# Performance work log

Hardware: AMD Instinct MI355X
Metric: run time of the kernel (lower is better)

## Reference

```python
import jax, jax.numpy as jnp
import numpy as np

B = 8192   # batch
S = 16     # n_dims = len(dims_in)
E = 256    # embedding_dim
H = 8      # heads
FF = 1024  # feedforward_dim
L = 6      # transformer_layers
V = 512    # max_dim (vocab per slot)
U = 1024   # mlp_units
DC = 64    # dims_c
LN_EPS = 1e-5


def setup_inputs() -> dict:
    key = jax.random.key(0)
    ks = iter(jax.random.split(key, 40))
    s = 0.02
    def p(shape):
        return jax.random.normal(next(ks), shape, jnp.float32) * s
    return dict(
        x=jax.random.randint(next(ks), (B, S), 0, V, dtype=jnp.int32),
        c=jax.random.normal(next(ks), (B, DC), jnp.float32),
        x_emb=p((V, E)),
        pos_emb=p((S, E)),
        c_W=p((E, DC)), c_b=jnp.zeros((E,), jnp.float32),
        Wqkv=p((L, 3 * E, E)), bqkv=jnp.zeros((L, 3 * E), jnp.float32),
        Wo=p((L, E, E)), bo=jnp.zeros((L, E), jnp.float32),
        ln1_g=jnp.ones((L, E), jnp.float32), ln1_b=jnp.zeros((L, E), jnp.float32),
        W1=p((L, FF, E)), b1=jnp.zeros((L, FF), jnp.float32),
        W2=p((L, E, FF)), b2=jnp.zeros((L, E), jnp.float32),
        ln2_g=jnp.ones((L, E), jnp.float32), ln2_b=jnp.zeros((L, E), jnp.float32),
        mW0=p((U, E)), mb0=jnp.zeros((U,), jnp.float32),
        mW1=p((U, U)), mb1=jnp.zeros((U,), jnp.float32),
        mW2=p((V, U)), mb2=jnp.zeros((V,), jnp.float32),
    )


def _ln(x, g, b):
    mu = x.mean(-1, keepdims=True)
    var = ((x - mu) ** 2).mean(-1, keepdims=True)
    return (x - mu) * jax.lax.rsqrt(var + LN_EPS) * g + b


def reference(x, c, x_emb, pos_emb, c_W, c_b, Wqkv, bqkv, Wo, bo,
              ln1_g, ln1_b, W1, b1, W2, b2, ln2_g, ln2_b,
              mW0, mb0, mW1, mb1, mW2, mb2):
    Bn = x.shape[0]
    dh = E // H
    # x_embed = pad(x_embedding(x[:, :-1]), one zero timestep at front)
    xe = jnp.pad(x_emb[x[:, :-1]], ((0, 0), (1, 0), (0, 0)))  # [B,S,E]
    h = xe + pos_emb[None] + (c @ c_W.T + c_b)[:, None, :]
    causal = jnp.triu(jnp.ones((S, S), bool), 1)  # True = masked
    for l in range(L):  # post-norm TransformerEncoderLayer, dropout=0, gelu
        qkv = h @ Wqkv[l].T + bqkv[l]
        q, k, v = jnp.split(qkv, 3, axis=-1)
        q = q.reshape(Bn, S, H, dh)
        k = k.reshape(Bn, S, H, dh)
        v = v.reshape(Bn, S, H, dh)
        sc = jnp.einsum('bshd,bthd->bhst', q, k) / np.sqrt(dh).astype(np.float32)
        sc = jnp.where(causal[None, None], jnp.float32(-1e30), sc)
        a = jax.nn.softmax(sc, axis=-1)
        o = jnp.einsum('bhst,bthd->bshd', a, v).reshape(Bn, S, E)
        h = _ln(h + o @ Wo[l].T + bo[l], ln1_g[l], ln1_b[l])
        f = jax.nn.gelu(h @ W1[l].T + b1[l], approximate=False) @ W2[l].T + b2[l]
        h = _ln(h + f, ln2_g[l], ln2_b[l])
    # MLP head: 3 linear layers with ReLU
    z = jax.nn.relu(h @ mW0.T + mb0)
    z = jax.nn.relu(z @ mW1.T + mb1)
    logits = z @ mW2.T + mb2  # [B,S,V]
    # prior_mask is all ones since dims_in[i] == max_dim for all i
    pu = jnp.exp(logits)
    picked = jnp.take_along_axis(pu, x[:, :, None], axis=2)[:, :, 0]
    prob = jnp.prod(picked / pu.sum(axis=2), axis=1)
    return jnp.log(prob)
```

## Files before the change

### kernel.cpp

```cpp
#include <hip/hip_runtime.h>
#include <hip/hip_bf16.h>
#include <math.h>

#define B_  8192
#define S_  16
#define E_  256
#define H_  8
#define FF_ 1024
#define L_  6
#define V_  512
#define U_  1024
#define DC_ 64
#define M_  (B_ * S_)

typedef __attribute__((ext_vector_type(8))) short short8;
typedef __attribute__((ext_vector_type(4))) float f32x4;

__device__ __forceinline__ float wave_sum(float v) {
#pragma unroll
  for (int off = 32; off >= 1; off >>= 1) v += __shfl_xor(v, off);
  return v;
}
__device__ __forceinline__ float wave_max(float v) {
#pragma unroll
  for (int off = 32; off >= 1; off >>= 1) v = fmaxf(v, __shfl_xor(v, off));
  return v;
}

__device__ __forceinline__ unsigned bfround(float f) {
  unsigned u = __builtin_bit_cast(unsigned, f);
  return (u + 0x7FFFu + ((u >> 16) & 1u)) >> 16;
}
__device__ __forceinline__ unsigned pack2(float lo, float hi) {
  return bfround(lo) | (bfround(hi) << 16);
}
__device__ __forceinline__ float b2f(short s) {
  return __builtin_bit_cast(float, (unsigned)(unsigned short)s << 16);
}
__device__ __forceinline__ float blo(unsigned u) { return __builtin_bit_cast(float, u << 16); }
__device__ __forceinline__ float bhi(unsigned u) { return __builtin_bit_cast(float, u & 0xFFFF0000u); }

__device__ __forceinline__ void gload_lds16(const void* g, void* l) {
  __builtin_amdgcn_global_load_lds(
      (const __attribute__((address_space(1))) void*)g,
      (__attribute__((address_space(3))) void*)l, 16, 0, 0);
}

__device__ __forceinline__ int xcd_swz(int bid, int nblk) {
  return (bid & 7) * (nblk >> 3) + (bid >> 3);
}

__global__ void w2bf_kernel(const float* __restrict__ src, short* __restrict__ dst) {
  const int i = blockIdx.x * 256 + threadIdx.x;
  const float4 v = ((const float4*)src)[i];
  uint2 p;
  p.x = pack2(v.x, v.y);
  p.y = pack2(v.z, v.w);
  ((uint2*)dst)[i] = p;
}

template <int ACT, bool RES, bool OUTF32>
__launch_bounds__(256, 2)
__global__ void gemm_bf16_kernel(const short* __restrict__ A, const short* __restrict__ W,
                                 const float* __restrict__ bias, const short* __restrict__ res,
                                 void* __restrict__ Cv, int M, int N, int K) {
  __shared__ __align__(16) short As[128 * 64];
  __shared__ __align__(16) short Ws[128 * 64];
  const int t  = threadIdx.x;
  const int w  = t >> 6;
  const int l  = t & 63;
  const int wr = w >> 1;
  const int wc = w & 1;
  const int lr = l & 15;
  const int kg = l >> 4;
  const int nbn = N / 128;
  const int bid = xcd_swz(blockIdx.x, gridDim.x);
  const int bm = bid / nbn;
  const int bn = bid % nbn;
  const int m0 = bm * 128, n0 = bn * 128;

  f32x4 acc[4][4] = {};

  const int rg = l >> 3;
  const int cs = ((l & 7) ^ rg) * 8;
  const int swz = (lr & 7) * 8;

  for (int k0 = 0; k0 < K; k0 += 64) {
    const short* Ab = &A[(size_t)m0 * K + k0 + cs];
    const short* Wb = &W[(size_t)n0 * K + k0 + cs];
#pragma unroll
    for (int q = 0; q < 4; ++q) {
      const int i = w * 4 + q;
      const int row = i * 8 + rg;
      gload_lds16(Ab + (size_t)row * K, &As[i * 512]);
      gload_lds16(Wb + (size_t)row * K, &Ws[i * 512]);
    }
    __syncthreads();

#pragma unroll
    for (int kk = 0; kk < 64; kk += 32) {
      short8 af[4], bf[4];
#pragma unroll
      for (int mi = 0; mi < 4; ++mi)
        af[mi] = *(const short8*)&As[(wr * 64 + mi * 16 + lr) * 64 + ((kk + kg * 8) ^ swz)];
#pragma unroll
      for (int ni = 0; ni < 4; ++ni)
        bf[ni] = *(const short8*)&Ws[(wc * 64 + ni * 16 + lr) * 64 + ((kk + kg * 8) ^ swz)];
#pragma unroll
      for (int mi = 0; mi < 4; ++mi)
#pragma unroll
        for (int ni = 0; ni < 4; ++ni)
          acc[mi][ni] = __builtin_amdgcn_mfma_f32_16x16x32_bf16(af[mi], bf[ni], acc[mi][ni], 0, 0, 0);
    }
    __syncthreads();
  }

  float* Cf = (float*)Cv;
  short* Cb = (short*)Cv;
#pragma unroll
  for (int ni = 0; ni < 4; ++ni) {
    const int n = n0 + wc * 64 + ni * 16 + lr;
    const float bv = bias[n];
#pragma unroll
    for (int mi = 0; mi < 4; ++mi) {
      const int mbase = m0 + wr * 64 + mi * 16 + kg * 4;
#pragma unroll
      for (int j = 0; j < 4; ++j) {
        float z = acc[mi][ni][j] + bv;
        const size_t off = (size_t)(mbase + j) * N + n;
        if (RES) z += b2f(res[off]);
        if (ACT == 1) z = 0.5f * z * (1.0f + erff(z * 0.70710678118654752f));
        if (ACT == 2) z = fmaxf(z, 0.0f);
        if (OUTF32) Cf[off] = z;
        else        Cb[off] = (short)bfround(z);
      }
    }
  }
}

__launch_bounds__(256, 2)
__global__ void gemm_ln_kernel(const short* __restrict__ A, const short* __restrict__ W,
                               const float* __restrict__ bias, const short* __restrict__ res,
                               const float* __restrict__ g, const float* __restrict__ bb,
                               short* __restrict__ out, int M, int K) {
  __shared__ __align__(16) short As[64 * 64];
  __shared__ __align__(16) short Ws[256 * 64];
  __shared__ float lnbuf[64][2][2];
  const int t  = threadIdx.x;
  const int w  = t >> 6;
  const int l  = t & 63;
  const int wr = w >> 1;
  const int wc = w & 1;
  const int lr = l & 15;
  const int kg = l >> 4;
  const int bid = xcd_swz(blockIdx.x, gridDim.x);
  const int m0 = bid * 64;

  f32x4 acc[2][8] = {};

  const int rg = l >> 3;
  const int cs = ((l & 7) ^ rg) * 8;
  const int swz = (lr & 7) * 8;

  for (int k0 = 0; k0 < K; k0 += 64) {
    const short* Ab = &A[(size_t)m0 * K + k0 + cs];
    const short* Wb = &W[(size_t)0 * K + k0 + cs];
#pragma unroll
    for (int q = 0; q < 2; ++q) {
      const int i = w * 2 + q;
      gload_lds16(Ab + (size_t)(i * 8 + rg) * K, &As[i * 512]);
    }
#pragma unroll
    for (int q = 0; q < 8; ++q) {
      const int i = w * 8 + q;
      gload_lds16(Wb + (size_t)(i * 8 + rg) * K, &Ws[i * 512]);
    }
    __syncthreads();

#pragma unroll
    for (int kk = 0; kk < 64; kk += 32) {
      short8 af[2], bf[8];
#pragma unroll
      for (int mi = 0; mi < 2; ++mi)
        af[mi] = *(const short8*)&As[(wr * 32 + mi * 16 + lr) * 64 + ((kk + kg * 8) ^ swz)];
#pragma unroll
      for (int ni = 0; ni < 8; ++ni)
        bf[ni] = *(const short8*)&Ws[(wc * 128 + ni * 16 + lr) * 64 + ((kk + kg * 8) ^ swz)];
#pragma unroll
      for (int mi = 0; mi < 2; ++mi)
#pragma unroll
        for (int ni = 0; ni < 8; ++ni)
          acc[mi][ni] = __builtin_amdgcn_mfma_f32_16x16x32_bf16(af[mi], bf[ni], acc[mi][ni], 0, 0, 0);
    }
    __syncthreads();
  }

  float biasv[8], gv[8], bv[8];
#pragma unroll
  for (int ni = 0; ni < 8; ++ni) {
    const int n = wc * 128 + ni * 16 + lr;
    biasv[ni] = bias[n]; gv[ni] = g[n]; bv[ni] = bb[n];
  }
  float ps1[2][4] = {}, ps2[2][4] = {};
#pragma unroll
  for (int mi = 0; mi < 2; ++mi)
#pragma unroll
    for (int j = 0; j < 4; ++j) {
      const int m = m0 + wr * 32 + mi * 16 + kg * 4 + j;
#pragma unroll
      for (int ni = 0; ni < 8; ++ni) {
        const int n = wc * 128 + ni * 16 + lr;
        float z = acc[mi][ni][j] + biasv[ni] + b2f(res[(size_t)m * 256 + n]);
        acc[mi][ni][j] = z;
        ps1[mi][j] += z;
        ps2[mi][j] = fmaf(z, z, ps2[mi][j]);
      }
    }
#pragma unroll
  for (int off = 1; off <= 8; off <<= 1) {
#pragma unroll
    for (int mi = 0; mi < 2; ++mi)
#pragma unroll
      for (int j = 0; j < 4; ++j) {
        ps1[mi][j] += __shfl_xor(ps1[mi][j], off);
        ps2[mi][j] += __shfl_xor(ps2[mi][j], off);
      }
  }
  if (lr == 0) {
#pragma unroll
    for (int mi = 0; mi < 2; ++mi)
#pragma unroll
      for (int j = 0; j < 4; ++j) {
        const int r = wr * 32 + mi * 16 + kg * 4 + j;
        lnbuf[r][wc][0] = ps1[mi][j];
        lnbuf[r][wc][1] = ps2[mi][j];
      }
  }
  __syncthreads();

#pragma unroll
  for (int mi = 0; mi < 2; ++mi)
#pragma unroll
    for (int j = 0; j < 4; ++j) {
      const int r = wr * 32 + mi * 16 + kg * 4 + j;
      const float s1 = lnbuf[r][0][0] + lnbuf[r][1][0];
      const float s2 = lnbuf[r][0][1] + lnbuf[r][1][1];
      const float mu  = s1 * (1.0f / 256.0f);
      const float var = s2 * (1.0f / 256.0f) - mu * mu;
      const float rs  = 1.0f / sqrtf(var + 1e-5f);
      const size_t mrow = (size_t)(m0 + r) * 256;
#pragma unroll
      for (int ni = 0; ni < 8; ++ni) {
        const int n = wc * 128 + ni * 16 + lr;
        out[mrow + n] = (short)bfround((acc[mi][ni][j] - mu) * rs * gv[ni] + bv[ni]);
      }
    }
}

__global__ void embed_kernel(const int* __restrict__ x, const float* __restrict__ x_emb,
                             const float* __restrict__ pos_emb, const float* __restrict__ cproj,
                             short* __restrict__ h, int b0) {
  const int idx = blockIdx.x * 256 + threadIdx.x;
  const int e4 = idx & 63;
  const int s  = (idx >> 6) & 15;
  const int b  = b0 + (idx >> 10);
  const float4 pe = ((const float4*)pos_emb)[s * 64 + e4];
  const float4 cp = ((const float4*)cproj)[b * 64 + e4];
  float4 v;
  v.x = pe.x + cp.x; v.y = pe.y + cp.y; v.z = pe.z + cp.z; v.w = pe.w + cp.w;
  if (s > 0) {
    const int tok = x[b * 16 + s - 1];
    const float4 xe = ((const float4*)x_emb)[tok * 64 + e4];
    v.x += xe.x; v.y += xe.y; v.z += xe.z; v.w += xe.w;
  }
  uint2 p;
  p.x = pack2(v.x, v.y);
  p.y = pack2(v.z, v.w);
  ((uint2*)h)[idx] = p;
}

__launch_bounds__(256)
__global__ void attn_kernel(const short* __restrict__ qkv, short* __restrict__ o) {
  __shared__ __align__(16) float sq[4][16][36];
  __shared__ __align__(16) float sk[4][16][36];
  __shared__ __align__(16) float sv[4][16][36];
  __shared__ float sa[4][16][17];
  const int w   = threadIdx.x >> 6;
  const int l   = threadIdx.x & 63;
  const int gid = blockIdx.x * 4 + w;
  const int b   = gid >> 3;
  const int hh  = gid & 7;

  {
    const int s  = l >> 2;
    const int d0 = (l & 3) * 8;
    const size_t base = (size_t)(b * 16 + s) * 768 + hh * 32 + d0;
    const uint4 qv = *(const uint4*)&qkv[base];
    const uint4 kv = *(const uint4*)&qkv[base + 256];
    const uint4 vv = *(const uint4*)&qkv[base + 512];
    float* dq = &sq[w][s][d0];
    float* dk = &sk[w][s][d0];
    float* dv = &sv[w][s][d0];
    dq[0] = blo(qv.x); dq[1] = bhi(qv.x); dq[2] = blo(qv.y); dq[3] = bhi(qv.y);
    dq[4] = blo(qv.z); dq[5] = bhi(qv.z); dq[6] = blo(qv.w); dq[7] = bhi(qv.w);
    dk[0] = blo(kv.x); dk[1] = bhi(kv.x); dk[2] = blo(kv.y); dk[3] = bhi(kv.y);
    dk[4] = blo(kv.z); dk[5] = bhi(kv.z); dk[6] = blo(kv.w); dk[7] = bhi(kv.w);
    dv[0] = blo(vv.x); dv[1] = bhi(vv.x); dv[2] = blo(vv.y); dv[3] = bhi(vv.y);
    dv[4] = blo(vv.z); dv[5] = bhi(vv.z); dv[6] = blo(vv.w); dv[7] = bhi(vv.w);
  }
  __syncthreads();

  {
    const int sr = l & 15;
    const int tq = l >> 4;
    float sc[4] = {0.f, 0.f, 0.f, 0.f};
    for (int d = 0; d < 32; d += 4) {
      const float4 qv = *(const float4*)&sq[w][sr][d];
#pragma unroll
      for (int j = 0; j < 4; ++j) {
        const float4 kv = *(const float4*)&sk[w][tq * 4 + j][d];
        sc[j] += qv.x * kv.x + qv.y * kv.y + qv.z * kv.z + qv.w * kv.w;
      }
    }
    float mx = -1e30f;
#pragma unroll
    for (int j = 0; j < 4; ++j) {
      const int tt = tq * 4 + j;
      sc[j] = (tt > sr) ? -1e30f : sc[j] * 0.17677669529663687f;
      mx = fmaxf(mx, sc[j]);
    }
    mx = fmaxf(mx, __shfl_xor(mx, 16));
    mx = fmaxf(mx, __shfl_xor(mx, 32));
    float e[4]; float sm = 0.f;
#pragma unroll
    for (int j = 0; j < 4; ++j) { e[j] = expf(sc[j] - mx); sm += e[j]; }
    sm += __shfl_xor(sm, 16);
    sm += __shfl_xor(sm, 32);
#pragma unroll
    for (int j = 0; j < 4; ++j) sa[w][sr][tq * 4 + j] = e[j] / sm;
  }
  __syncthreads();

  {
    const int s  = l >> 2;
    const int d0 = (l & 3) * 8;
    float a0[4] = {0.f, 0.f, 0.f, 0.f}, a1[4] = {0.f, 0.f, 0.f, 0.f};
    for (int tt = 0; tt < 16; ++tt) {
      const float av = sa[w][s][tt];
      const float4 v0 = *(const float4*)&sv[w][tt][d0];
      const float4 v1 = *(const float4*)&sv[w][tt][d0 + 4];
      a0[0] = fmaf(av, v0.x, a0[0]); a0[1] = fmaf(av, v0.y, a0[1]);
      a0[2] = fmaf(av, v0.z, a0[2]); a0[3] = fmaf(av, v0.w, a0[3]);
      a1[0] = fmaf(av, v1.x, a1[0]); a1[1] = fmaf(av, v1.y, a1[1]);
      a1[2] = fmaf(av, v1.z, a1[2]); a1[3] = fmaf(av, v1.w, a1[3]);
    }
    const size_t ob = (size_t)(b * 16 + s) * 256 + hh * 32 + d0;
    uint4 p;
    p.x = pack2(a0[0], a0[1]); p.y = pack2(a0[2], a0[3]);
    p.z = pack2(a1[0], a1[1]); p.w = pack2(a1[2], a1[3]);
    *(uint4*)&o[ob] = p;
  }
}

__launch_bounds__(256)
__global__ void logprob_kernel(const float* __restrict__ logits, const int* __restrict__ x,
                               float* __restrict__ out, int b0) {
  const int w  = threadIdx.x >> 6;
  const int l  = threadIdx.x & 63;
  const int bl = blockIdx.x * 4 + w;
  const int b  = b0 + bl;
  float acc = 0.f;
  for (int s = 0; s < 16; ++s) {
    const float* row = logits + (size_t)(bl * 16 + s) * 512;
    float v[8];
#pragma unroll
    for (int i = 0; i < 8; ++i) v[i] = row[l + 64 * i];
    float mx = v[0];
#pragma unroll
    for (int i = 1; i < 8; ++i) mx = fmaxf(mx, v[i]);
    mx = wave_max(mx);
    float se = 0.f;
#pragma unroll
    for (int i = 0; i < 8; ++i) se += expf(v[i] - mx);
    se = wave_sum(se);
    const float lse = mx + logf(se);
    const float picked = row[x[b * 16 + s]];
    acc += picked - lse;
  }
  if (l == 0) out[b] = acc;
}

extern "C" void kernel_launch(void* const* d_in, const int* in_sizes, int n_in,
                              void* d_out, int out_size, void* d_ws, size_t ws_size,
                              hipStream_t stream) {
  const int*   x       = (const int*)  d_in[0];
  const float* c       = (const float*)d_in[1];
  const float* x_emb   = (const float*)d_in[2];
  const float* pos_emb = (const float*)d_in[3];
  const float* c_W     = (const float*)d_in[4];
  const float* c_b     = (const float*)d_in[5];
  const float* Wqkv    = (const float*)d_in[6];
  const float* bqkv    = (const float*)d_in[7];
  const float* Wo      = (const float*)d_in[8];
  const float* bo      = (const float*)d_in[9];
  const float* ln1_g   = (const float*)d_in[10];
  const float* ln1_b   = (const float*)d_in[11];
  const float* W1      = (const float*)d_in[12];
  const float* b1      = (const float*)d_in[13];
  const float* W2      = (const float*)d_in[14];
  const float* b2      = (const float*)d_in[15];
  const float* ln2_g   = (const float*)d_in[16];
  const float* ln2_b   = (const float*)d_in[17];
  const float* mW0     = (const float*)d_in[18];
  const float* mb0     = (const float*)d_in[19];
  const float* mW1     = (const float*)d_in[20];
  const float* mb1     = (const float*)d_in[21];
  const float* mW2     = (const float*)d_in[22];
  const float* mb2     = (const float*)d_in[23];
  float* out = (float*)d_out;

  const size_t nWqkv = (size_t)L_ * 768 * 256;
  const size_t nWo   = (size_t)L_ * 256 * 256;
  const size_t nW1   = (size_t)L_ * 1024 * 256;
  const size_t nW2   = (size_t)L_ * 256 * 1024;
  const size_t nmW0  = (size_t)U_ * E_;
  const size_t nmW1  = (size_t)U_ * U_;
  const size_t nmW2  = (size_t)V_ * U_;
  const size_t ncW   = (size_t)E_ * DC_;
  const size_t nC    = (size_t)B_ * DC_;
  const size_t WBF   = nWqkv + nWo + nW1 + nW2 + nmW0 + nmW1 + nmW2 + ncW + nC;

  short* bWqkv = (short*)d_ws;
  short* bWo   = bWqkv + nWqkv;
  short* bW1   = bWo   + nWo;
  short* bW2   = bW1   + nW1;
  short* bmW0  = bW2   + nW2;
  short* bmW1  = bmW0  + nmW0;
  short* bmW2  = bmW1  + nmW1;
  short* bcW   = bmW2  + nmW2;
  short* bC    = bcW   + ncW;

  const size_t fixed_bytes = WBF * 2 + (size_t)B_ * 256 * 4;
  int BC = 0;
  for (int bc = B_; bc >= 128; bc >>= 1) {
    const size_t need = fixed_bytes + (size_t)bc * 16 * 2304 * 2;
    if (need <= ws_size) { BC = bc; break; }
  }
  if (BC == 0) return;
  const int MC = BC * 16;
  const int NCHUNK = B_ / BC;

  float* cpr = (float*)((char*)d_ws + WBF * 2);
  short* h   = (short*)(cpr + (size_t)B_ * 256);
  short* R   = h + (size_t)MC * 256;
  short* X   = R + (size_t)MC * 1024;
  float* logitsF = (float*)R;

  const dim3 blk(256);

  w2bf_kernel<<<dim3(nWqkv / 1024), blk, 0, stream>>>(Wqkv, bWqkv);
  w2bf_kernel<<<dim3(nWo   / 1024), blk, 0, stream>>>(Wo,   bWo);
  w2bf_kernel<<<dim3(nW1   / 1024), blk, 0, stream>>>(W1,   bW1);
  w2bf_kernel<<<dim3(nW2   / 1024), blk, 0, stream>>>(W2,   bW2);
  w2bf_kernel<<<dim3(nmW0  / 1024), blk, 0, stream>>>(mW0,  bmW0);
  w2bf_kernel<<<dim3(nmW1  / 1024), blk, 0, stream>>>(mW1,  bmW1);
  w2bf_kernel<<<dim3(nmW2  / 1024), blk, 0, stream>>>(mW2,  bmW2);
  w2bf_kernel<<<dim3(ncW   / 1024), blk, 0, stream>>>(c_W,  bcW);
  w2bf_kernel<<<dim3(nC    / 1024), blk, 0, stream>>>(c,    bC);

  gemm_bf16_kernel<0, false, true><<<dim3((B_ / 128) * (E_ / 128)), blk, 0, stream>>>(
      bC, bcW, c_b, nullptr, cpr, B_, E_, DC_);

  for (int ci = 0; ci < NCHUNK; ++ci) {
    const int b0 = ci * BC;
    embed_kernel<<<dim3((MC * 64) / 256), blk, 0, stream>>>(x, x_emb, pos_emb, cpr, h, b0);

    for (int l = 0; l < L_; ++l) {
      gemm_bf16_kernel<0, false, false><<<dim3((MC / 128) * (768 / 128)), blk, 0, stream>>>(
          h, bWqkv + (size_t)l * 768 * 256, bqkv + (size_t)l * 768, nullptr, R, MC, 768, 256);
      attn_kernel<<<dim3(BC * 2), blk, 0, stream>>>(R, X);
      gemm_ln_kernel<<<dim3(MC / 64), blk, 0, stream>>>(
          X, bWo + (size_t)l * 256 * 256, bo + (size_t)l * 256, h,
          ln1_g + (size_t)l * 256, ln1_b + (size_t)l * 256, h, MC, 256);
      gemm_bf16_kernel<1, false, false><<<dim3((MC / 128) * (FF_ / 128)), blk, 0, stream>>>(
          h, bW1 + (size_t)l * 1024 * 256, b1 + (size_t)l * 1024, nullptr, R, MC, 1024, 256);
      gemm_ln_kernel<<<dim3(MC / 64), blk, 0, stream>>>(
          R, bW2 + (size_t)l * 256 * 1024, b2 + (size_t)l * 256, h,
          ln2_g + (size_t)l * 256, ln2_b + (size_t)l * 256, h, MC, 1024);
    }

    gemm_bf16_kernel<2, false, false><<<dim3((MC / 128) * (U_ / 128)), blk, 0, stream>>>(
        h, bmW0, mb0, nullptr, R, MC, U_, E_);
    gemm_bf16_kernel<2, false, false><<<dim3((MC / 128) * (U_ / 128)), blk, 0, stream>>>(
        R, bmW1, mb1, nullptr, X, MC, U_, U_);
    gemm_bf16_kernel<0, false, true><<<dim3((MC / 128) * (V_ / 128)), blk, 0, stream>>>(
        X, bmW2, mb2, nullptr, logitsF, MC, V_, U_);

    logprob_kernel<<<dim3(BC / 4), blk, 0, stream>>>(logitsF, x, out, b0);
  }
}
```

Baseline: 3.841 ms.

## Fuse causal attention into the Wo projection + residual + LayerNorm kernel

Attention for a 64-row tile (4 sequences, all 8 heads) is now computed in shared memory inside the output-projection GEMM kernel. The per-head outputs are written into a swizzled LDS buffer that feeds the MFMA loop directly. This removes a separate attention launch and the global round-trip of the attention output tensor. In exchange, the attention phase runs head by head with three block barriers per head, and the LDS footprint grows, which may limit occupancy.

```diff
diff --git a/kernel.cpp b/kernel.cpp
--- a/kernel.cpp
+++ b/kernel.cpp
@@ -257,6 +257,200 @@
     }
 }
 
+__launch_bounds__(256, 2)
+__global__ void attn_wo_ln_kernel(const short* __restrict__ qkv, const short* __restrict__ W,
+                                  const float* __restrict__ bias, const short* __restrict__ res,
+                                  const float* __restrict__ g, const float* __restrict__ bb,
+                                  short* __restrict__ out, int M) {
+  __shared__ __align__(16) short oS[64 * 256];
+  __shared__ __align__(16) short Ws[256 * 64];
+  __shared__ float lnbuf[64][2][2];
+  const int t  = threadIdx.x;
+  const int w  = t >> 6;
+  const int l  = t & 63;
+  const int wr = w >> 1;
+  const int wc = w & 1;
+  const int lr = l & 15;
+  const int kg = l >> 4;
+  const int bid = xcd_swz(blockIdx.x, gridDim.x);
+  const int m0 = bid * 64;
+
+  {
+    float* scr = (float*)Ws;
+    float* sq = scr + w * 2048;
+    float* sk = sq + 576;
+    float* sv = sq + 1152;
+    float* sa = sq + 1728;
+    const int s  = l >> 2;
+    const int d0 = (l & 3) * 8;
+    const int sr = l & 15;
+    const int tq = l >> 4;
+
+    for (int hh = 0; hh < 8; ++hh) {
+      {
+        const size_t base = (size_t)(m0 + w * 16 + s) * 768 + hh * 32 + d0;
+        const uint4 qv = *(const uint4*)&qkv[base];
+        const uint4 kv = *(const uint4*)&qkv[base + 256];
+        const uint4 vv = *(const uint4*)&qkv[base + 512];
+        float* dq = &sq[s * 36 + d0];
+        float* dk = &sk[s * 36 + d0];
+        float* dv = &sv[s * 36 + d0];
+        dq[0] = blo(qv.x); dq[1] = bhi(qv.x); dq[2] = blo(qv.y); dq[3] = bhi(qv.y);
+        dq[4] = blo(qv.z); dq[5] = bhi(qv.z); dq[6] = blo(qv.w); dq[7] = bhi(qv.w);
+        dk[0] = blo(kv.x); dk[1] = bhi(kv.x); dk[2] = blo(kv.y); dk[3] = bhi(kv.y);
+        dk[4] = blo(kv.z); dk[5] = bhi(kv.z); dk[6] = blo(kv.w); dk[7] = bhi(kv.w);
+        dv[0] = blo(vv.x); dv[1] = bhi(vv.x); dv[2] = blo(vv.y); dv[3] = bhi(vv.y);
+        dv[4] = blo(vv.z); dv[5] = bhi(vv.z); dv[6] = blo(vv.w); dv[7] = bhi(vv.w);
+      }
+      __syncthreads();
+      {
+        float sc[4] = {0.f, 0.f, 0.f, 0.f};
+        for (int d = 0; d < 32; d += 4) {
+          const float4 qv = *(const float4*)&sq[sr * 36 + d];
+#pragma unroll
+          for (int j = 0; j < 4; ++j) {
+            const float4 kv = *(const float4*)&sk[(tq * 4 + j) * 36 + d];
+            sc[j] += qv.x * kv.x + qv.y * kv.y + qv.z * kv.z + qv.w * kv.w;
+          }
+        }
+        float mx = -1e30f;
+#pragma unroll
+        for (int j = 0; j < 4; ++j) {
+          const int tt = tq * 4 + j;
+          sc[j] = (tt > sr) ? -1e30f : sc[j] * 0.17677669529663687f;
+          mx = fmaxf(mx, sc[j]);
+        }
+        mx = fmaxf(mx, __shfl_xor(mx, 16));
+        mx = fmaxf(mx, __shfl_xor(mx, 32));
+        float e[4]; float sm = 0.f;
+#pragma unroll
+        for (int j = 0; j < 4; ++j) { e[j] = expf(sc[j] - mx); sm += e[j]; }
+        sm += __shfl_xor(sm, 16);
+        sm += __shfl_xor(sm, 32);
+#pragma unroll
+        for (int j = 0; j < 4; ++j) sa[sr * 17 + tq * 4 + j] = e[j] / sm;
+      }
+      __syncthreads();
+      {
+        float a0[4] = {0.f, 0.f, 0.f, 0.f}, a1[4] = {0.f, 0.f, 0.f, 0.f};
+        for (int tt = 0; tt < 16; ++tt) {
+          const float av = sa[s * 17 + tt];
+          const float4 v0 = *(const float4*)&sv[tt * 36 + d0];
+          const float4 v1 = *(const float4*)&sv[tt * 36 + d0 + 4];
+          a0[0] = fmaf(av, v0.x, a0[0]); a0[1] = fmaf(av, v0.y, a0[1]);
+          a0[2] = fmaf(av, v0.z, a0[2]); a0[3] = fmaf(av, v0.w, a0[3]);
+          a1[0] = fmaf(av, v1.x, a1[0]); a1[1] = fmaf(av, v1.y, a1[1]);
+          a1[2] = fmaf(av, v1.z, a1[2]); a1[3] = fmaf(av, v1.w, a1[3]);
+        }
+        const int r = w * 16 + s;
+        const int cphys = (hh * 32 + d0) ^ ((r & 7) * 8);
+        uint4 p;
+        p.x = pack2(a0[0], a0[1]); p.y = pack2(a0[2], a0[3]);
+        p.z = pack2(a1[0], a1[1]); p.w = pack2(a1[2], a1[3]);
+        *(uint4*)&oS[r * 256 + cphys] = p;
+      }
+      __syncthreads();
+    }
+  }
+
+  f32x4 acc[2][8] = {};
+  const int rg = l >> 3;
+  const int cs = ((l & 7) ^ rg) * 8;
+  const int swz = (lr & 7) * 8;
+  const int ar0 = wr * 32 + lr;
+
+  for (int k0 = 0; k0 < 256; k0 += 64) {
+    const short* Wb = &W[(size_t)0 * 256 + k0 + cs];
+#pragma unroll
+    for (int q = 0; q < 8; ++q) {
+      const int i = w * 8 + q;
+      gload_lds16(Wb + (size_t)(i * 8 + rg) * 256, &Ws[i * 512]);
+    }
+    __syncthreads();
+
+#pragma unroll
+    for (int kk = 0; kk < 64; kk += 32) {
+      short8 af[2], bf[8];
+#pragma unroll
+      for (int mi = 0; mi < 2; ++mi) {
+        const int row = ar0 + mi * 16;
+        const int col = k0 + kk + kg * 8;
+        af[mi] = *(const short8*)&oS[row * 256 + (col ^ ((row & 7) * 8))];
+      }
+#pragma unroll
+      for (int ni = 0; ni < 8; ++ni)
+        bf[ni] = *(const short8*)&Ws[(wc * 128 + ni * 16 + lr) * 64 + ((kk + kg * 8) ^ swz)];
+#pragma unroll
+      for (int mi = 0; mi < 2; ++mi)
+#pragma unroll
+        for (int ni = 0; ni < 8; ++ni)
+          acc[mi][ni] = __builtin_amdgcn_mfma_f32_16x16x32_bf16(af[mi], bf[ni], acc[mi][ni], 0, 0, 0);
+    }
+    __syncthreads();
+  }
+
+  float biasv[8], gv[8], bv[8];
+#pragma unroll
+  for (int ni = 0; ni < 8; ++ni) {
+    const int n = wc * 128 + ni * 16 + lr;
+    biasv[ni] = bias[n]; gv[ni] = g[n]; bv[ni] = bb[n];
+  }
+  float ps1[2][4] = {}, ps2[2][4] = {};
+#pragma unroll
+  for (int mi = 0; mi < 2; ++mi)
+#pragma unroll
+    for (int j = 0; j < 4; ++j) {
+      const int m = m0 + wr * 32 + mi * 16 + kg * 4 + j;
+#pragma unroll
+      for (int ni = 0; ni < 8; ++ni) {
+        const int n = wc * 128 + ni * 16 + lr;
+        float z = acc[mi][ni][j] + biasv[ni] + b2f(res[(size_t)m * 256 + n]);
+        acc[mi][ni][j] = z;
+        ps1[mi][j] += z;
+        ps2[mi][j] = fmaf(z, z, ps2[mi][j]);
+      }
+    }
+#pragma unroll
+  for (int off = 1; off <= 8; off <<= 1) {
+#pragma unroll
+    for (int mi = 0; mi < 2; ++mi)
+#pragma unroll
+      for (int j = 0; j < 4; ++j) {
+        ps1[mi][j] += __shfl_xor(ps1[mi][j], off);
+        ps2[mi][j] += __shfl_xor(ps2[mi][j], off);
+      }
+  }
+  if (lr == 0) {
+#pragma unroll
+    for (int mi = 0; mi < 2; ++mi)
+#pragma unroll
+      for (int j = 0; j < 4; ++j) {
+        const int r = wr * 32 + mi * 16 + kg * 4 + j;
+        lnbuf[r][wc][0] = ps1[mi][j];
+        lnbuf[r][wc][1] = ps2[mi][j];
+      }
+  }
+  __syncthreads();
+
+#pragma unroll
+  for (int mi = 0; mi < 2; ++mi)
+#pragma unroll
+    for (int j = 0; j < 4; ++j) {
+      const int r = wr * 32 + mi * 16 + kg * 4 + j;
+      const float s1 = lnbuf[r][0][0] + lnbuf[r][1][0];
+      const float s2 = lnbuf[r][0][1] + lnbuf[r][1][1];
+      const float mu  = s1 * (1.0f / 256.0f);
+      const float var = s2 * (1.0f / 256.0f) - mu * mu;
+      const float rs  = 1.0f / sqrtf(var + 1e-5f);
+      const size_t mrow = (size_t)(m0 + r) * 256;
+#pragma unroll
+      for (int ni = 0; ni < 8; ++ni) {
+        const int n = wc * 128 + ni * 16 + lr;
+        out[mrow + n] = (short)bfround((acc[mi][ni][j] - mu) * rs * gv[ni] + bv[ni]);
+      }
+    }
+}
+
 __global__ void embed_kernel(const int* __restrict__ x, const float* __restrict__ x_emb,
                              const float* __restrict__ pos_emb, const float* __restrict__ cproj,
                              short* __restrict__ h, int b0) {
@@ -277,89 +471,6 @@
   p.x = pack2(v.x, v.y);
   p.y = pack2(v.z, v.w);
   ((uint2*)h)[idx] = p;
-}
-
-__launch_bounds__(256)
-__global__ void attn_kernel(const short* __restrict__ qkv, short* __restrict__ o) {
-  __shared__ __align__(16) float sq[4][16][36];
-  __shared__ __align__(16) float sk[4][16][36];
-  __shared__ __align__(16) float sv[4][16][36];
-  __shared__ float sa[4][16][17];
-  const int w   = threadIdx.x >> 6;
-  const int l   = threadIdx.x & 63;
-  const int gid = blockIdx.x * 4 + w;
-  const int b   = gid >> 3;
-  const int hh  = gid & 7;
-
-  {
-    const int s  = l >> 2;
-    const int d0 = (l & 3) * 8;
-    const size_t base = (size_t)(b * 16 + s) * 768 + hh * 32 + d0;
-    const uint4 qv = *(const uint4*)&qkv[base];
-    const uint4 kv = *(const uint4*)&qkv[base + 256];
-    const uint4 vv = *(const uint4*)&qkv[base + 512];
-    float* dq = &sq[w][s][d0];
-    float* dk = &sk[w][s][d0];
-    float* dv = &sv[w][s][d0];
-    dq[0] = blo(qv.x); dq[1] = bhi(qv.x); dq[2] = blo(qv.y); dq[3] = bhi(qv.y);
-    dq[4] = blo(qv.z); dq[5] = bhi(qv.z); dq[6] = blo(qv.w); dq[7] = bhi(qv.w);
-    dk[0] = blo(kv.x); dk[1] = bhi(kv.x); dk[2] = blo(kv.y); dk[3] = bhi(kv.y);
-    dk[4] = blo(kv.z); dk[5] = bhi(kv.z); dk[6] = blo(kv.w); dk[7] = bhi(kv.w);
-    dv[0] = blo(vv.x); dv[1] = bhi(vv.x); dv[2] = blo(vv.y); dv[3] = bhi(vv.y);
-    dv[4] = blo(vv.z); dv[5] = bhi(vv.z); dv[6] = blo(vv.w); dv[7] = bhi(vv.w);
-  }
-  __syncthreads();
-
-  {
-    const int sr = l & 15;
-    const int tq = l >> 4;
-    float sc[4] = {0.f, 0.f, 0.f, 0.f};
-    for (int d = 0; d < 32; d += 4) {
-      const float4 qv = *(const float4*)&sq[w][sr][d];
-#pragma unroll
-      for (int j = 0; j < 4; ++j) {
-        const float4 kv = *(const float4*)&sk[w][tq * 4 + j][d];
-        sc[j] += qv.x * kv.x + qv.y * kv.y + qv.z * kv.z + qv.w * kv.w;
-      }
-    }
-    float mx = -1e30f;
-#pragma unroll
-    for (int j = 0; j < 4; ++j) {
-      const int tt = tq * 4 + j;
-      sc[j] = (tt > sr) ? -1e30f : sc[j] * 0.17677669529663687f;
-      mx = fmaxf(mx, sc[j]);
-    }
-    mx = fmaxf(mx, __shfl_xor(mx, 16));
-    mx = fmaxf(mx, __shfl_xor(mx, 32));
-    float e[4]; float sm = 0.f;
-#pragma unroll
-    for (int j = 0; j < 4; ++j) { e[j] = expf(sc[j] - mx); sm += e[j]; }
-    sm += __shfl_xor(sm, 16);
-    sm += __shfl_xor(sm, 32);
-#pragma unroll
-    for (int j = 0; j < 4; ++j) sa[w][sr][tq * 4 + j] = e[j] / sm;
-  }
-  __syncthreads();
-
-  {
-    const int s  = l >> 2;
-    const int d0 = (l & 3) * 8;
-    float a0[4] = {0.f, 0.f, 0.f, 0.f}, a1[4] = {0.f, 0.f, 0.f, 0.f};
-    for (int tt = 0; tt < 16; ++tt) {
-      const float av = sa[w][s][tt];
-      const float4 v0 = *(const float4*)&sv[w][tt][d0];
-      const float4 v1 = *(const float4*)&sv[w][tt][d0 + 4];
-      a0[0] = fmaf(av, v0.x, a0[0]); a0[1] = fmaf(av, v0.y, a0[1]);
-      a0[2] = fmaf(av, v0.z, a0[2]); a0[3] = fmaf(av, v0.w, a0[3]);
-      a1[0] = fmaf(av, v1.x, a1[0]); a1[1] = fmaf(av, v1.y, a1[1]);
-      a1[2] = fmaf(av, v1.z, a1[2]); a1[3] = fmaf(av, v1.w, a1[3]);
-    }
-    const size_t ob = (size_t)(b * 16 + s) * 256 + hh * 32 + d0;
-    uint4 p;
-    p.x = pack2(a0[0], a0[1]); p.y = pack2(a0[2], a0[3]);
-    p.z = pack2(a1[0], a1[1]); p.w = pack2(a1[2], a1[3]);
-    *(uint4*)&o[ob] = p;
-  }
 }
 
 __launch_bounds__(256)
@@ -478,10 +589,9 @@
     for (int l = 0; l < L_; ++l) {
       gemm_bf16_kernel<0, false, false><<<dim3((MC / 128) * (768 / 128)), blk, 0, stream>>>(
           h, bWqkv + (size_t)l * 768 * 256, bqkv + (size_t)l * 768, nullptr, R, MC, 768, 256);
-      attn_kernel<<<dim3(BC * 2), blk, 0, stream>>>(R, X);
-      gemm_ln_kernel<<<dim3(MC / 64), blk, 0, stream>>>(
-          X, bWo + (size_t)l * 256 * 256, bo + (size_t)l * 256, h,
-          ln1_g + (size_t)l * 256, ln1_b + (size_t)l * 256, h, MC, 256);
+      attn_wo_ln_kernel<<<dim3(MC / 64), blk, 0, stream>>>(
+          R, bWo + (size_t)l * 256 * 256, bo + (size_t)l * 256, h,
+          ln1_g + (size_t)l * 256, ln1_b + (size_t)l * 256, h, MC);
       gemm_bf16_kernel<1, false, false><<<dim3((MC / 128) * (FF_ / 128)), blk, 0, stream>>>(
           h, bW1 + (size_t)l * 1024 * 256, b1 + (size_t)l * 1024, nullptr, R, MC, 1024, 256);
       gemm_ln_kernel<<<dim3(MC / 64), blk, 0, stream>>>(
```

Result: slower. 3.922 ms (+2.1%).

## Fuse final logits GEMM with log-softmax and token pick

Applied to the files above, without the earlier changes.

Replaces the final V=512 output GEMM plus separate logprob kernel with a single kernel. Each block computes 64 rows across two 256-column halves and keeps an online max/sum-exp per row in shared memory, so the fp32 logits never go to global memory. The cost is that each block re-streams the full 512x1024 weight matrix with 64-row tiles, giving less weight reuse than the 128x128 GEMM tiles. The epilogue also adds several block-wide syncs.

```diff
diff --git a/kernel.cpp b/kernel.cpp
--- a/kernel.cpp
+++ b/kernel.cpp
@@ -257,6 +257,141 @@
     }
 }
 
+__launch_bounds__(256, 2)
+__global__ void gemm_lp_kernel(const short* __restrict__ A, const short* __restrict__ W,
+                               const float* __restrict__ bias, const int* __restrict__ x,
+                               float* __restrict__ out, int b0) {
+  __shared__ __align__(16) short As[64 * 64];
+  __shared__ __align__(16) short Ws[256 * 64];
+  __shared__ float redm[64][2];
+  __shared__ float reds[64][2];
+  __shared__ float run_m[64], run_s[64], pickb[64];
+  __shared__ int   xb[64];
+  const int t  = threadIdx.x;
+  const int w  = t >> 6;
+  const int l  = t & 63;
+  const int wr = w >> 1;
+  const int wc = w & 1;
+  const int lr = l & 15;
+  const int kg = l >> 4;
+  const int bid = xcd_swz(blockIdx.x, gridDim.x);
+  const int m0 = bid * 64;
+
+  if (t < 64) {
+    xb[t]   = x[(size_t)b0 * 16 + m0 + t];
+    run_m[t] = -1e30f;
+    run_s[t] = 0.f;
+  }
+  __syncthreads();
+
+  const int rg = l >> 3;
+  const int cs = ((l & 7) ^ rg) * 8;
+  const int swz = (lr & 7) * 8;
+
+  for (int half = 0; half < 2; ++half) {
+    f32x4 acc[2][8] = {};
+    for (int k0 = 0; k0 < 1024; k0 += 64) {
+      const short* Ab = &A[(size_t)m0 * 1024 + k0 + cs];
+      const short* Wb = &W[(size_t)(half * 256) * 1024 + k0 + cs];
+#pragma unroll
+      for (int q = 0; q < 2; ++q) {
+        const int i = w * 2 + q;
+        gload_lds16(Ab + (size_t)(i * 8 + rg) * 1024, &As[i * 512]);
+      }
+#pragma unroll
+      for (int q = 0; q < 8; ++q) {
+        const int i = w * 8 + q;
+        gload_lds16(Wb + (size_t)(i * 8 + rg) * 1024, &Ws[i * 512]);
+      }
+      __syncthreads();
+#pragma unroll
+      for (int kk = 0; kk < 64; kk += 32) {
+        short8 af[2], bf[8];
+#pragma unroll
+        for (int mi = 0; mi < 2; ++mi)
+          af[mi] = *(const short8*)&As[(wr * 32 + mi * 16 + lr) * 64 + ((kk + kg * 8) ^ swz)];
+#pragma unroll
+        for (int ni = 0; ni < 8; ++ni)
+          bf[ni] = *(const short8*)&Ws[(wc * 128 + ni * 16 + lr) * 64 + ((kk + kg * 8) ^ swz)];
+#pragma unroll
+        for (int mi = 0; mi < 2; ++mi)
+#pragma unroll
+          for (int ni = 0; ni < 8; ++ni)
+            acc[mi][ni] = __builtin_amdgcn_mfma_f32_16x16x32_bf16(af[mi], bf[ni], acc[mi][ni], 0, 0, 0);
+      }
+      __syncthreads();
+    }
+
+    float bv[8];
+#pragma unroll
+    for (int ni = 0; ni < 8; ++ni)
+      bv[ni] = bias[half * 256 + wc * 128 + ni * 16 + lr];
+#pragma unroll
+    for (int mi = 0; mi < 2; ++mi)
+#pragma unroll
+      for (int j = 0; j < 4; ++j) {
+        float pm = -1e30f;
+#pragma unroll
+        for (int ni = 0; ni < 8; ++ni) {
+          const float z = acc[mi][ni][j] + bv[ni];
+          acc[mi][ni][j] = z;
+          pm = fmaxf(pm, z);
+        }
+#pragma unroll
+        for (int off = 1; off <= 8; off <<= 1) pm = fmaxf(pm, __shfl_xor(pm, off));
+        if (lr == 0) redm[wr * 32 + mi * 16 + kg * 4 + j][wc] = pm;
+      }
+    __syncthreads();
+
+#pragma unroll
+    for (int mi = 0; mi < 2; ++mi)
+#pragma unroll
+      for (int j = 0; j < 4; ++j) {
+        const int r  = wr * 32 + mi * 16 + kg * 4 + j;
+        const float rm = fmaxf(redm[r][0], redm[r][1]);
+        const int  xv = xb[r];
+        float ps = 0.f;
+#pragma unroll
+        for (int ni = 0; ni < 8; ++ni) {
+          const float z = acc[mi][ni][j];
+          ps += expf(z - rm);
+          const int col = half * 256 + wc * 128 + ni * 16 + lr;
+          if (col == xv) pickb[r] = z;
+        }
+#pragma unroll
+        for (int off = 1; off <= 8; off <<= 1) ps += __shfl_xor(ps, off);
+        if (lr == 0) reds[r][wc] = ps;
+      }
+    __syncthreads();
+
+    if (wc == 0 && lr == 0) {
+#pragma unroll
+      for (int mi = 0; mi < 2; ++mi)
+#pragma unroll
+        for (int j = 0; j < 4; ++j) {
+          const int r = wr * 32 + mi * 16 + kg * 4 + j;
+          const float m1 = fmaxf(redm[r][0], redm[r][1]);
+          const float s1 = reds[r][0] + reds[r][1];
+          const float mo = run_m[r];
+          const float mn = fmaxf(mo, m1);
+          run_s[r] = run_s[r] * expf(mo - mn) + s1 * expf(m1 - mn);
+          run_m[r] = mn;
+        }
+    }
+    __syncthreads();
+  }
+
+  if (t < 4) {
+    float lp = 0.f;
+#pragma unroll
+    for (int s = 0; s < 16; ++s) {
+      const int r = t * 16 + s;
+      lp += pickb[r] - (run_m[r] + logf(run_s[r]));
+    }
+    out[b0 + (m0 >> 4) + t] = lp;
+  }
+}
+
 __global__ void embed_kernel(const int* __restrict__ x, const float* __restrict__ x_emb,
                              const float* __restrict__ pos_emb, const float* __restrict__ cproj,
                              short* __restrict__ h, int b0) {
@@ -360,34 +495,6 @@
     p.z = pack2(a1[0], a1[1]); p.w = pack2(a1[2], a1[3]);
     *(uint4*)&o[ob] = p;
   }
-}
-
-__launch_bounds__(256)
-__global__ void logprob_kernel(const float* __restrict__ logits, const int* __restrict__ x,
-                               float* __restrict__ out, int b0) {
-  const int w  = threadIdx.x >> 6;
-  const int l  = threadIdx.x & 63;
-  const int bl = blockIdx.x * 4 + w;
-  const int b  = b0 + bl;
-  float acc = 0.f;
-  for (int s = 0; s < 16; ++s) {
-    const float* row = logits + (size_t)(bl * 16 + s) * 512;
-    float v[8];
-#pragma unroll
-    for (int i = 0; i < 8; ++i) v[i] = row[l + 64 * i];
-    float mx = v[0];
-#pragma unroll
-    for (int i = 1; i < 8; ++i) mx = fmaxf(mx, v[i]);
-    mx = wave_max(mx);
-    float se = 0.f;
-#pragma unroll
-    for (int i = 0; i < 8; ++i) se += expf(v[i] - mx);
-    se = wave_sum(se);
-    const float lse = mx + logf(se);
-    const float picked = row[x[b * 16 + s]];
-    acc += picked - lse;
-  }
-  if (l == 0) out[b] = acc;
 }
 
 extern "C" void kernel_launch(void* const* d_in, const int* in_sizes, int n_in,
@@ -454,7 +561,6 @@
   short* h   = (short*)(cpr + (size_t)B_ * 256);
   short* R   = h + (size_t)MC * 256;
   short* X   = R + (size_t)MC * 1024;
-  float* logitsF = (float*)R;
 
   const dim3 blk(256);
 
@@ -493,9 +599,6 @@
         h, bmW0, mb0, nullptr, R, MC, U_, E_);
     gemm_bf16_kernel<2, false, false><<<dim3((MC / 128) * (U_ / 128)), blk, 0, stream>>>(
         R, bmW1, mb1, nullptr, X, MC, U_, U_);
-    gemm_bf16_kernel<0, false, true><<<dim3((MC / 128) * (V_ / 128)), blk, 0, stream>>>(
-        X, bmW2, mb2, nullptr, logitsF, MC, V_, U_);
-
-    logprob_kernel<<<dim3(BC / 4), blk, 0, stream>>>(logitsF, x, out, b0);
-  }
-}
+    gemm_lp_kernel<<<dim3(MC / 64), blk, 0, stream>>>(X, bmW2, mb2, x, out, b0);
+  }
+}
```

After: 3.640 ms. -5.2%, faster.
